# Performance work log

Measured on AMD Instinct MI355X. Metric: run time of the kernel, lower is better.

Reference implementation:

```python
import jax, jax.numpy as jnp
import numpy as np
import jax.scipy.linalg as jsl
from jax import lax

N_SAMPLES = 16384
N_COMPONENTS = 16
N_FEATURES = 128
EPS = 1e-3
MAX_DEPTH = 8
JITTER = 1e-6
LOG_2PI = float(np.log(2.0 * np.pi))


def _em_update(x, means, covs):
    # One call of update_parameters(): weights are (un-normalized) mahalanobis
    # distances computed with the OLD means/covariances; diffs for the
    # covariance update also use the OLD means (diff is computed before the
    # in-place mean assignment in the torch code).
    d = x.shape[1]
    inv = jnp.linalg.inv(covs)                      # [K,D,D]
    diff = x[:, None, :] - means[None, :, :]        # [N,K,D]
    sol = jnp.einsum('kde,nke->nkd', inv, diff)     # [N,K,D]
    w = jnp.einsum('nkd,nkd->nk', diff, sol)        # [N,K] mahalanobis dists
    sw = w.sum(axis=0)                              # [K]
    new_means = jnp.einsum('nk,nd->kd', w, x) / sw[:, None]
    outer = jnp.einsum('nk,nkd,nke->kde', w, diff, diff)
    new_covs = outer / sw[:, None, None] + JITTER * jnp.eye(d, dtype=x.dtype)
    return new_means, new_covs


def _em_loop(x, means, covs):
    # Faithful to the torch while-loop: update first, then check convergence
    # of the means (Frobenius norm) against eps, up to max_depth iterations.
    def cond(c):
        _, _, _, depth, done = c
        return jnp.logical_and(depth < MAX_DEPTH, jnp.logical_not(done))

    def body(c):
        m, cv, prev, depth, _ = c
        nm, nc = _em_update(x, m, cv)
        diff = jnp.linalg.norm(nm - prev)
        done = diff <= EPS
        return (nm, nc, nm, depth + 1, done)

    init = (means, covs, means, jnp.int32(0), jnp.bool_(False))
    m, cv, _, _, _ = lax.while_loop(cond, body, init)
    return m, cv


def _log_prob(x, means, covs):
    # MultivariateNormal.log_prob for each component, batched over K via
    # Cholesky (matching torch.distributions internals).
    d = x.shape[1]
    L = jnp.linalg.cholesky(covs)                   # [K,D,D]
    diff = x[:, None, :] - means[None, :, :]        # [N,K,D]
    # per-component triangular solve: L_k y = diff[:,k,:]^T -> y [K,D,N]
    y = jax.vmap(lambda Lk, dk: jsl.solve_triangular(Lk, dk.T, lower=True),
                 in_axes=(0, 1))(L, diff)
    maha = jnp.sum(y * y, axis=1)                   # [K,N]
    logdet = 2.0 * jnp.sum(jnp.log(jnp.diagonal(L, axis1=-2, axis2=-1)), axis=-1)  # [K]
    return -0.5 * (d * LOG_2PI + logdet[:, None] + maha)  # [K,N]


def _forward(x, means, covariances, weights):
    # torch.no_grad() EM loop -> stop_gradient on loop inputs/outputs
    m0 = lax.stop_gradient(means)
    c0 = lax.stop_gradient(covariances)
    xs = lax.stop_gradient(x)
    m_loop, c_loop = _em_loop(xs, m0, c0)
    # final update_parameters call (training path, outside no_grad)
    m_fin, c_fin = _em_update(x, m_loop, c_loop)
    logp = _log_prob(x, m_fin, c_fin)               # [K,N]
    loss = -jnp.sum(weights[:, None] * logp)
    return loss, m_fin, c_fin


def setup_inputs() -> dict:
    key = jax.random.key(0)
    k1, k2 = jax.random.split(key)
    x = jax.random.normal(k1, (N_SAMPLES, N_FEATURES), dtype=jnp.float32)
    means = jax.random.normal(k2, (N_COMPONENTS, N_FEATURES), dtype=jnp.float32)
    covariances = jnp.tile(jnp.eye(N_FEATURES, dtype=jnp.float32),
                           (N_COMPONENTS, 1, 1))
    weights = jnp.ones((N_COMPONENTS,), jnp.float32) / N_COMPONENTS
    return {"x": x, "means": means, "covariances": covariances,
            "weights": weights}


def reference(x, means, covariances, weights):
    return _forward(x, means, covariances, weights)
```

## Files before the change

kernel.cpp:

```cpp
#include <hip/hip_runtime.h>
#include <math.h>


#define NS 16384
#define DD 128
#define KC 16
#define JITTER_ 1e-6f
#define EPS2_ 1e-6f
#define LOG_2PI_ 1.8378770664093454f
#define NCHUNK 1024

typedef __attribute__((ext_vector_type(8))) short bf16x8;
typedef __attribute__((ext_vector_type(16))) float f32x16;

enum : int {
  OFF_CUR_M  = 0,
  OFF_CS     = 2048,
  OFF_T      = 528384,
  OFF_LOGDET = 530432,
  OFF_SW     = 530448,
  OFF_NUM    = 530464,
  OFF_W      = 532512,
  OFF_LOSSK  = 794656,
  OFF_DIFFSQ = 794672,
  OFF_DONE   = 794673,
  OFF_CTR    = 794674,
  OFF_XAH    = 794676,
  OFF_XAL    = 1843252,
  OFF_XBH    = 2891828,
  OFF_XBL    = 3940404,
  OFF_LBH    = 4988980,
  OFF_LBL    = 5120052,
  WS_FLOATS  = 5251124
};

__device__ __forceinline__ float bf2f(ushort u) {
  union { unsigned u; float f; } c; c.u = ((unsigned)u) << 16; return c.f;
}
__device__ __forceinline__ ushort f2bf_rne(float f) {
  union { float f; unsigned u; } c; c.f = f;
  unsigned r = c.u + 0x7fffu + ((c.u >> 16) & 1u);
  return (ushort)(r >> 16);
}
__device__ __forceinline__ ushort f2bf_trunc(float f) {
  union { float f; unsigned u; } c; c.f = f; return (ushort)(c.u >> 16);
}

__device__ __forceinline__ int swz(int r, int c) {
  return (r << 7) + ((((c >> 2) + r) & 31) << 2) + (c & 3);
}

__device__ __forceinline__ float rdlane(float v, int lane) {
  union { float f; int i; } c; c.f = v;
  c.i = __builtin_amdgcn_readlane(c.i, lane);
  return c.f;
}

__device__ __forceinline__ void frag_write(const float* Zs, ushort* LBH,
                                           ushort* LBL, int g) {
  int ll = g & 63, ks2 = (g >> 6) & 1, ec = (g >> 7) & 3, dg = (g >> 9) & 3;
  int d = 32 * dg + (ll & 31);
  int e = 32 * ec + 16 * ks2 + 8 * (ll >> 5);
  float4 z0 = *(const float4*)&Zs[d * 132 + e];
  float4 z1 = *(const float4*)&Zs[d * 132 + e + 4];
  float zv[8] = {z0.x, z0.y, z0.z, z0.w, z1.x, z1.y, z1.z, z1.w};
  ushort hh[8], lo2[8];
  #pragma unroll
  for (int j = 0; j < 8; ++j) {
    hh[j]  = f2bf_trunc(zv[j]);
    lo2[j] = f2bf_rne(zv[j] - bf2f(hh[j]));
  }
  *(ushort4*)&LBH[g * 8]     = make_ushort4(hh[0], hh[1], hh[2], hh[3]);
  *(ushort4*)&LBH[g * 8 + 4] = make_ushort4(hh[4], hh[5], hh[6], hh[7]);
  *(ushort4*)&LBL[g * 8]     = make_ushort4(lo2[0], lo2[1], lo2[2], lo2[3]);
  *(ushort4*)&LBL[g * 8 + 4] = make_ushort4(lo2[4], lo2[5], lo2[6], lo2[7]);
}

__global__ __launch_bounds__(256) void k_init_split(const float* __restrict__ x,
                                                    const float* __restrict__ means,
                                                    const float* __restrict__ covs,
                                                    float* __restrict__ ws) {
  __shared__ float xt[64 * 132];
  int b = blockIdx.x, t = threadIdx.x;
  int idx = b * 256 + t;
  for (int i = idx; i < KC * DD * DD; i += 256 * 256) ws[OFF_CS + i] = covs[i];
  if (idx < KC * DD) ws[OFF_CUR_M + idx] = means[idx];
  if (idx == 0) {
    ws[OFF_DIFFSQ] = 0.f;
    ((int*)ws)[OFF_DONE] = 0;
    ((int*)ws)[OFF_CTR]  = 0;
  }
  int n0 = b * 64;
  for (int fi = t; fi < 2048; fi += 256) {
    int n = fi >> 5, q = (fi & 31) * 4;
    *(float4*)&xt[n * 132 + q] = *(const float4*)&x[(size_t)(n0 + n) * DD + q];
  }
  __syncthreads();
  ushort* __restrict__ XAH = (ushort*)(ws + OFF_XAH);
  ushort* __restrict__ XAL = (ushort*)(ws + OFF_XAL);
  ushort* __restrict__ XBH = (ushort*)(ws + OFF_XBH);
  ushort* __restrict__ XBL = (ushort*)(ws + OFF_XBL);
  for (int s = t; s < 1024; s += 256) {
    int l = s & 63, ks = (s >> 6) & 1, ec = (s >> 7) & 3, ngl = (s >> 9) & 1;
    int nl = 32 * ngl + (l & 31);
    int e0 = 32 * ec + 16 * ks + 8 * (l >> 5);
    float vv[8];
    *(float4*)&vv[0] = *(const float4*)&xt[nl * 132 + e0];
    *(float4*)&vv[4] = *(const float4*)&xt[nl * 132 + e0 + 4];
    ushort h[8], lo[8];
    #pragma unroll
    for (int j = 0; j < 8; ++j) {
      h[j]  = f2bf_trunc(vv[j]);
      lo[j] = f2bf_rne(vv[j] - bf2f(h[j]));
    }
    size_t base = ((((size_t)((n0 >> 5) + ngl) * 4 + ec) * 2 + ks) * 64 + l) * 8;
    *(ushort4*)&XAH[base]     = make_ushort4(h[0], h[1], h[2], h[3]);
    *(ushort4*)&XAH[base + 4] = make_ushort4(h[4], h[5], h[6], h[7]);
    *(ushort4*)&XAL[base]     = make_ushort4(lo[0], lo[1], lo[2], lo[3]);
    *(ushort4*)&XAL[base + 4] = make_ushort4(lo[4], lo[5], lo[6], lo[7]);
  }
  for (int s = t; s < 1024; s += 256) {
    int l = s & 63, nbl = (s >> 6) & 3, eg = (s >> 8) & 3;
    int e = 32 * eg + (l & 31);
    int nl = 16 * nbl + 8 * (l >> 5);
    ushort h[8], lo[8];
    #pragma unroll
    for (int j = 0; j < 8; ++j) {
      float v = xt[(nl + j) * 132 + e];
      h[j]  = f2bf_trunc(v);
      lo[j] = f2bf_rne(v - bf2f(h[j]));
    }
    size_t base = (((size_t)eg * (NS / 16) + (n0 >> 4) + nbl) * 64 + l) * 8;
    *(ushort4*)&XBH[base]     = make_ushort4(h[0], h[1], h[2], h[3]);
    *(ushort4*)&XBH[base + 4] = make_ushort4(h[4], h[5], h[6], h[7]);
    *(ushort4*)&XBL[base]     = make_ushort4(lo[0], lo[1], lo[2], lo[3]);
    *(ushort4*)&XBL[base + 4] = make_ushort4(lo[4], lo[5], lo[6], lo[7]);
  }
}

__global__ __launch_bounds__(512) void k_fused(float* __restrict__ ws, float* __restrict__ dout,
                                               int guarded, int do_update, int write_out,
                                               int accum_diff, int final_pass) {
  if (guarded && ((const int*)ws)[OFF_DONE]) return;
  __shared__ float m[DD * DD];
  __shared__ float Zs[DD * 132];
  __shared__ float Ws[64 * 68];
  __shared__ float invd_s[DD];
  __shared__ float cm_s[DD], nm_s[DD];
  __shared__ float redbuf[2];
  int k = blockIdx.x, t = threadIdx.x;
  int l = t & 63, wv = t >> 6;
  float* __restrict__ CS = ws + OFF_CS + (size_t)k * DD * DD;

  if (do_update) {
    float sw = ws[OFF_SW + k];
    float inv = 1.f / sw;
    float4 s4v[8];
    #pragma unroll
    for (int it = 0; it < 8; ++it)
      s4v[it] = *(const float4*)&CS[(it * 512 + t) * 4];
    if (t < DD) {
      cm_s[t] = ws[OFF_CUR_M + k * DD + t];
      nm_s[t] = ws[OFF_NUM + k * DD + t];
    }
    __syncthreads();
    float* __restrict__ doutC = dout + 1 + KC * DD + (size_t)k * DD * DD;
    #pragma unroll
    for (int it = 0; it < 8; ++it) {
      int idx = (it * 512 + t) * 4;
      float4 s4 = s4v[it];
      int d = idx >> 7, e = idx & 127;
      float md = cm_s[d], nd = nm_s[d];
      float4 me4 = *(const float4*)&cm_s[e];
      float4 ne4 = *(const float4*)&nm_s[e];
      float4 v;
      v.x = (s4.x - md * ne4.x - nd * me4.x + sw * md * me4.x) * inv;
      v.y = (s4.y - md * ne4.y - nd * me4.y + sw * md * me4.y) * inv;
      v.z = (s4.z - md * ne4.z - nd * me4.z + sw * md * me4.z) * inv;
      v.w = (s4.w - md * ne4.w - nd * me4.w + sw * md * me4.w) * inv;
      if (d >= e && d < e + 4) (&v.x)[d - e] += JITTER_;
      *(float4*)&m[swz(d, e)] = v;
      if (write_out) *(float4*)&doutC[idx] = v;
    }
    if (t < DD) {
      float me = cm_s[t], ne = nm_s[t];
      float newm = ne * inv;
      ws[OFF_CUR_M + k * DD + t] = newm;
      if (write_out) dout[1 + k * DD + t] = newm;
      if (accum_diff) {
        float dm = newm - me;
        float s = dm * dm;
        #pragma unroll
        for (int mk2 = 1; mk2 < 64; mk2 <<= 1) s += __shfl_xor(s, mk2, 64);
        if (l == 0) redbuf[wv] = s;
      }
      ws[OFF_NUM + k * DD + t] = 0.f;
    }
    if (t == 0) {
      ws[OFF_SW + k] = 0.f;
      if (final_pass) ws[OFF_LOSSK + k] = 0.f;
    }
  } else {
    #pragma unroll
    for (int it = 0; it < 8; ++it) {
      int idx = (it * 512 + t) * 4;
      float4 c4 = *(const float4*)&CS[idx];
      *(float4*)&m[swz(idx >> 7, idx & 127)] = c4;
    }
    if (t < DD) ws[OFF_NUM + k * DD + t] = 0.f;
    if (t == 0) ws[OFF_SW + k] = 0.f;
  }
  __syncthreads();

  auto FACTOR = [&](int P) {
    int ra = P + l, rb = P + 64 + l;
    bool isA = (wv == 0);
    bool va = ra < DD, vb = rb < DD;
    float A[16], B[16];
    if (va) {
      #pragma unroll
      for (int q = 0; q < 4; ++q) {
        float4 v = *(const float4*)&m[swz(ra, P + 4 * q)];
        A[4*q+0] = v.x; A[4*q+1] = v.y; A[4*q+2] = v.z; A[4*q+3] = v.w;
      }
    }
    if (!isA && vb) {
      #pragma unroll
      for (int q = 0; q < 4; ++q) {
        float4 v = *(const float4*)&m[swz(rb, P + 4 * q)];
        B[4*q+0] = v.x; B[4*q+1] = v.y; B[4*q+2] = v.z; B[4*q+3] = v.w;
      }
    }
    #pragma unroll
    for (int jj = 0; jj < 16; ++jj) {
      float dj = rdlane(A[jj], jj);
      float inv = __builtin_amdgcn_rsqf(dj);
      inv = inv * (1.5f - 0.5f * dj * inv * inv);
      float sj = dj * inv;
      if (va) {
        if (l == jj) A[jj] = sj;
        else if (l > jj) A[jj] *= inv;
      }
      if (!isA && vb) B[jj] *= inv;
      #pragma unroll
      for (int jj2 = jj + 1; jj2 < 16; ++jj2) {
        float c = rdlane(A[jj], jj2);
        if (va && l > jj) A[jj2] -= A[jj] * c;
        if (!isA && vb) B[jj2] -= B[jj] * c;
      }
    }
    if (isA && va) {
      #pragma unroll
      for (int q = 0; q < 4; ++q)
        *(float4*)&m[swz(ra, P + 4 * q)] = make_float4(A[4*q], A[4*q+1], A[4*q+2], A[4*q+3]);
    }
    if (!isA && vb) {
      #pragma unroll
      for (int q = 0; q < 4; ++q)
        *(float4*)&m[swz(rb, P + 4 * q)] = make_float4(B[4*q], B[4*q+1], B[4*q+2], B[4*q+3]);
    }
  };
  auto TILE16 = [&](int i0, int q0, int P) {
    float acc4[4][4] = {};
    #pragma unroll
    for (int pq = 0; pq < 4; ++pq) {
      float4 a[4], b[4];
      #pragma unroll
      for (int r = 0; r < 4; ++r) a[r] = *(const float4*)&m[swz(i0 + r, P + 4 * pq)];
      #pragma unroll
      for (int c = 0; c < 4; ++c) b[c] = *(const float4*)&m[swz(q0 + c, P + 4 * pq)];
      #pragma unroll
      for (int r = 0; r < 4; ++r)
        #pragma unroll
        for (int c = 0; c < 4; ++c)
          acc4[r][c] += a[r].x * b[c].x + a[r].y * b[c].y +
                        a[r].z * b[c].z + a[r].w * b[c].w;
    }
    #pragma unroll
    for (int r = 0; r < 4; ++r) {
      float4 v = *(const float4*)&m[swz(i0 + r, q0)];
      v.x -= acc4[r][0]; v.y -= acc4[r][1]; v.z -= acc4[r][2]; v.w -= acc4[r][3];
      *(float4*)&m[swz(i0 + r, q0)] = v;
    }
  };

  if (wv < 2) FACTOR(0);
  __syncthreads();
  for (int P = 0; P < DD - 16; P += 16) {
    int C0 = P + 16;
    int nts = DD - C0;
    for (int idx = t; idx < nts; idx += 512)
      TILE16(C0 + 4 * (idx >> 2), C0 + 4 * (idx & 3), P);
    __syncthreads();
    if (wv < 2) {
      FACTOR(C0);
    } else {
      int R0 = P + 32, s = DD - R0;
      if (s > 0) {
        int nt = s >> 2, tri = (nt * (nt + 1)) >> 1;
        for (int idx = t - 128; idx < tri; idx += 384) {
          int ti = (int)(0.5f * (sqrtf(8.f * (float)idx + 1.f) - 1.f));
          while (((ti + 1) * (ti + 2)) >> 1 <= idx) ++ti;
          while ((ti * (ti + 1)) >> 1 > idx) --ti;
          int tj = idx - ((ti * (ti + 1)) >> 1);
          TILE16(R0 + 4 * ti, R0 + 4 * tj, P);
        }
      }
    }
    __syncthreads();
  }

  if (t < DD) {
    float dv = m[swz(t, t)];
    invd_s[t] = 1.f / dv;
    if (final_pass) {
      float lg = logf(dv);
      #pragma unroll
      for (int mk2 = 1; mk2 < 64; mk2 <<= 1) lg += __shfl_xor(lg, mk2, 64);
      if (l == 0) redbuf[wv] = lg;
    }
  }
  __syncthreads();
  if (t < DD) {
    int b = t >> 5, j = t & 31, r0 = 32 * b;
    float acc[32];
    #pragma unroll
    for (int i2 = 0; i2 < 32; ++i2) acc[i2] = 0.f;
    #pragma unroll
    for (int p = 0; p < 32; ++p) {
      float zp = (((p == j) ? 1.f : 0.f) - acc[p]) * invd_s[r0 + p];
      Zs[(r0 + p) * 132 + r0 + j] = zp;
      #pragma unroll
      for (int i2 = p + 1; i2 < 32; ++i2)
        acc[i2] += m[swz(r0 + i2, r0 + p)] * zp;
    }
  } else {
    for (int z = t - 128; z < 1536; z += 384) {
      int r, c;
      if (z < 1024) { r = z >> 4; c = 64 + ((z & 15) << 2); }
      else { int z2 = z - 1024; int h = z2 >> 8; int z3 = z2 & 255;
             r = h * 64 + (z3 >> 3); c = h * 64 + 32 + ((z3 & 7) << 2); }
      *(float4*)&Zs[r * 132 + c] = make_float4(0.f, 0.f, 0.f, 0.f);
    }
    if (final_pass && t == 128) ws[OFF_LOGDET + k] = 2.f * (redbuf[0] + redbuf[1]);
  }
  __syncthreads();
  {
    int h = t >> 8, i = (t >> 3) & 31, j0 = (t & 7) << 2;
    int rI = h * 64 + 32 + i, cb = h * 64;
    float ax = 0.f, ay = 0.f, az = 0.f, aw = 0.f;
    #pragma unroll
    for (int q0 = 0; q0 < 32; q0 += 4) {
      float4 a  = *(const float4*)&m[swz(rI, cb + q0)];
      float4 z0 = *(const float4*)&Zs[(cb + q0 + 0) * 132 + cb + j0];
      float4 z1 = *(const float4*)&Zs[(cb + q0 + 1) * 132 + cb + j0];
      float4 z2 = *(const float4*)&Zs[(cb + q0 + 2) * 132 + cb + j0];
      float4 z3 = *(const float4*)&Zs[(cb + q0 + 3) * 132 + cb + j0];
      ax += a.x * z0.x + a.y * z1.x + a.z * z2.x + a.w * z3.x;
      ay += a.x * z0.y + a.y * z1.y + a.z * z2.y + a.w * z3.y;
      az += a.x * z0.z + a.y * z1.z + a.z * z2.z + a.w * z3.z;
      aw += a.x * z0.w + a.y * z1.w + a.z * z2.w + a.w * z3.w;
    }
    *(float4*)&Ws[(h * 32 + i) * 68 + j0] = make_float4(ax, ay, az, aw);
  }
  __syncthreads();
  {
    int h = t >> 8, i = (t >> 3) & 31, j0 = (t & 7) << 2;
    int rI = h * 64 + 32 + i;
    float ax = 0.f, ay = 0.f, az = 0.f, aw = 0.f;
    #pragma unroll
    for (int q0 = 0; q0 < 32; q0 += 4) {
      float4 a  = *(const float4*)&Zs[rI * 132 + h * 64 + 32 + q0];
      float4 w0 = *(const float4*)&Ws[(h * 32 + q0 + 0) * 68 + j0];
      float4 w1 = *(const float4*)&Ws[(h * 32 + q0 + 1) * 68 + j0];
      float4 w2 = *(const float4*)&Ws[(h * 32 + q0 + 2) * 68 + j0];
      float4 w3 = *(const float4*)&Ws[(h * 32 + q0 + 3) * 68 + j0];
      ax += a.x * w0.x + a.y * w1.x + a.z * w2.x + a.w * w3.x;
      ay += a.x * w0.y + a.y * w1.y + a.z * w2.y + a.w * w3.y;
      az += a.x * w0.z + a.y * w1.z + a.z * w2.z + a.w * w3.z;
      aw += a.x * w0.w + a.y * w1.w + a.z * w2.w + a.w * w3.w;
    }
    *(float4*)&Zs[rI * 132 + h * 64 + j0] = make_float4(-ax, -ay, -az, -aw);
  }
  __syncthreads();
  ushort* __restrict__ LBH = (ushort*)(ws + OFF_LBH) + (size_t)k * 16384;
  ushort* __restrict__ LBL = (ushort*)(ws + OFF_LBL) + (size_t)k * 16384;
  if (t < 256) {
    int i0 = (t & 15) << 2, j0 = (t >> 4) << 2;
    float acc4[4][4] = {};
    for (int q0 = 0; q0 < 64; q0 += 4) {
      float4 a[4], b[4];
      #pragma unroll
      for (int r = 0; r < 4; ++r) a[r] = *(const float4*)&m[swz(64 + i0 + r, q0)];
      #pragma unroll
      for (int s2 = 0; s2 < 4; ++s2) b[s2] = *(const float4*)&Zs[(q0 + s2) * 132 + j0];
      #pragma unroll
      for (int r = 0; r < 4; ++r) {
        acc4[r][0] += a[r].x * b[0].x + a[r].y * b[1].x + a[r].z * b[2].x + a[r].w * b[3].x;
        acc4[r][1] += a[r].x * b[0].y + a[r].y * b[1].y + a[r].z * b[2].y + a[r].w * b[3].y;
        acc4[r][2] += a[r].x * b[0].z + a[r].y * b[1].z + a[r].z * b[2].z + a[r].w * b[3].z;
        acc4[r][3] += a[r].x * b[0].w + a[r].y * b[1].w + a[r].z * b[2].w + a[r].w * b[3].w;
      }
    }
    #pragma unroll
    for (int r = 0; r < 4; ++r)
      *(float4*)&Ws[(i0 + r) * 68 + j0] =
          make_float4(acc4[r][0], acc4[r][1], acc4[r][2], acc4[r][3]);
  } else {
    #pragma unroll
    for (int it = 0; it < 3; ++it) frag_write(Zs, LBH, LBL, (t - 256) + it * 256);
  }
  __syncthreads();
  if (t < 256) {
    int i0 = (t & 15) << 2, j0 = (t >> 4) << 2;
    float acc4[4][4] = {};
    for (int q0 = 0; q0 < 64; q0 += 4) {
      float4 a[4], b[4];
      #pragma unroll
      for (int r = 0; r < 4; ++r)
        a[r] = *(const float4*)&Zs[(64 + i0 + r) * 132 + 64 + q0];
      #pragma unroll
      for (int s2 = 0; s2 < 4; ++s2) b[s2] = *(const float4*)&Ws[(q0 + s2) * 68 + j0];
      #pragma unroll
      for (int r = 0; r < 4; ++r) {
        acc4[r][0] += a[r].x * b[0].x + a[r].y * b[1].x + a[r].z * b[2].x + a[r].w * b[3].x;
        acc4[r][1] += a[r].x * b[0].y + a[r].y * b[1].y + a[r].z * b[2].y + a[r].w * b[3].y;
        acc4[r][2] += a[r].x * b[0].z + a[r].y * b[1].z + a[r].z * b[2].z + a[r].w * b[3].z;
        acc4[r][3] += a[r].x * b[0].w + a[r].y * b[1].w + a[r].z * b[2].w + a[r].w * b[3].w;
      }
    }
    #pragma unroll
    for (int r = 0; r < 4; ++r)
      *(float4*)&Zs[(64 + i0 + r) * 132 + j0] =
          make_float4(-acc4[r][0], -acc4[r][1], -acc4[r][2], -acc4[r][3]);
  } else {
    #pragma unroll
    for (int it = 0; it < 3; ++it) {
      int r = 768 + (t - 256) + it * 256;
      int g;
      if (r < 1024) g = r;
      else { int rr = r - 1024;
             g = (2 + (rr >> 8)) * 512 + (2 + ((rr >> 7) & 1)) * 128 + (rr & 127); }
      frag_write(Zs, LBH, LBL, g);
    }
  }
  __syncthreads();
  if (t < DD) {
    const float* __restrict__ mk = ws + OFF_CUR_M + k * DD;
    float s0 = 0.f;
    for (int e = 0; e < DD; e += 4) {
      float4 z = *(const float4*)&Zs[t * 132 + e];
      s0 += z.x * mk[e] + z.y * mk[e + 1] + z.z * mk[e + 2] + z.w * mk[e + 3];
    }
    ws[OFF_T + k * DD + t] = s0;
  } else {
    for (int rr = t - 128; rr < 512; rr += 384) {
      int g = (2 + (rr >> 8)) * 512 + ((rr >> 7) & 1) * 128 + (rr & 127);
      frag_write(Zs, LBH, LBL, g);
    }
  }
  if (accum_diff && t == 0) {
    atomicAdd(&ws[OFF_DIFFSQ], redbuf[0] + redbuf[1]);
    __threadfence();
    int old = atomicAdd((int*)ws + OFF_CTR, 1);
    if ((old & (KC - 1)) == KC - 1) {
      float v = atomicAdd(&ws[OFF_DIFFSQ], 0.f);
      if (v <= EPS2_) atomicExch((int*)ws + OFF_DONE, 1);
      atomicExch(&ws[OFF_DIFFSQ], 0.f);
    }
  }
}

__global__ __launch_bounds__(256) void k_quad(float* __restrict__ ws,
                                              const float* __restrict__ wts,
                                              int guarded, int final_pass) {
  if (guarded && ((const int*)ws)[OFF_DONE]) return;
  __shared__ float warr[128];
  int k = blockIdx.y, bx = blockIdx.x, t = threadIdx.x;
  int l = t & 63, wv = t >> 6;
  int n0 = bx * 128;
  if (t < 128) ws[OFF_CS + (size_t)k * DD * DD + bx * 128 + t] = 0.f;
  const ushort* __restrict__ XAH = (const ushort*)(ws + OFF_XAH);
  const ushort* __restrict__ XAL = (const ushort*)(ws + OFF_XAL);
  const ushort* __restrict__ LBH = (const ushort*)(ws + OFF_LBH) + (size_t)k * 16384;
  const ushort* __restrict__ LBL = (const ushort*)(ws + OFF_LBL) + (size_t)k * 16384;
  f32x16 acc[4] = {};
  size_t ng4 = (size_t)(4 * bx + wv) * 4;
  #pragma unroll
  for (int ec = 0; ec < 4; ++ec) {
    #pragma unroll
    for (int ks = 0; ks < 2; ++ks) {
      size_t aoff = (((ng4 + ec) * 2 + ks) * 64 + l) * 8;
      bf16x8 ah = *(const bf16x8*)&XAH[aoff];
      bf16x8 al = *(const bf16x8*)&XAL[aoff];
      #pragma unroll
      for (int dg = 0; dg < 4; ++dg) {
        size_t boff = ((((size_t)dg * 4 + ec) * 2 + ks) * 64 + l) * 8;
        bf16x8 bh = *(const bf16x8*)&LBH[boff];
        bf16x8 bl = *(const bf16x8*)&LBL[boff];
        acc[dg] = __builtin_amdgcn_mfma_f32_32x32x16_bf16(ah, bh, acc[dg], 0, 0, 0);
        acc[dg] = __builtin_amdgcn_mfma_f32_32x32x16_bf16(ah, bl, acc[dg], 0, 0, 0);
        acc[dg] = __builtin_amdgcn_mfma_f32_32x32x16_bf16(al, bh, acc[dg], 0, 0, 0);
      }
    }
  }
  float tv[4];
  #pragma unroll
  for (int c = 0; c < 4; ++c) tv[c] = ws[OFF_T + k * DD + 32 * c + (l & 31)];
  float part[16];
  #pragma unroll
  for (int r = 0; r < 16; ++r) {
    float s = 0.f;
    #pragma unroll
    for (int c = 0; c < 4; ++c) { float d = acc[c][r] - tv[c]; s += d * d; }
    part[r] = s;
  }
  #pragma unroll
  for (int mk2 = 1; mk2 < 32; mk2 <<= 1)
    #pragma unroll
    for (int r = 0; r < 16; ++r) part[r] += __shfl_xor(part[r], mk2, 64);
  int h = l >> 5;
  if ((l & 31) < 16) {
    int r = l & 31;
    int row = (r & 3) + 8 * (r >> 2) + 4 * h + 32 * wv;
    ws[OFF_W + k * NS + n0 + row] = part[r];
    if (final_pass) warr[row] = part[r];
  }
  if (final_pass) {
    __syncthreads();
    if (t < 64) {
      float s = warr[t] + warr[t + 64];
      #pragma unroll
      for (int mk2 = 1; mk2 < 64; mk2 <<= 1) s += __shfl_xor(s, mk2, 64);
      if (t == 0) atomicAdd(&ws[OFF_LOSSK + k], 0.5f * wts[k] * s);
    }
  }
}

__global__ __launch_bounds__(256, 4) void k_scatter(float* __restrict__ ws, int guarded) {
  if (guarded && ((const int*)ws)[OFF_DONE]) return;
  __shared__ float Sred[8192];
  int id = blockIdx.x, t = threadIdx.x;
  int xcd = id & 7, j = id >> 3;
  int chunk = xcd + 8 * (j & 1);
  int dg = (j >> 1) & 3;
  int k = j >> 3;
  int l = t & 63, wv = t >> 6;
  const ushort* __restrict__ XBH = (const ushort*)(ws + OFF_XBH);
  const ushort* __restrict__ XBL = (const ushort*)(ws + OFF_XBL);
  const float* __restrict__ wp = ws + OFF_W + k * NS + chunk * NCHUNK;
  f32x16 acc[4] = {};
  int nb0 = chunk * (NCHUNK / 16) + wv * (NCHUNK / 64);
  int ko = (l >> 5) * 8;
  float zsum = 0.f, wsum = 0.f;
  size_t aoff = (((size_t)dg * (NS / 16) + nb0) * 64 + l) * 8;
  bf16x8 th = *(const bf16x8*)&XBH[aoff];
  bf16x8 tl = *(const bf16x8*)&XBL[aoff];
  float4 w0 = *(const float4*)&wp[16 * (wv * (NCHUNK / 64)) + ko];
  float4 w1 = *(const float4*)&wp[16 * (wv * (NCHUNK / 64)) + ko + 4];
  for (int st = 0; st < NCHUNK / 64; ++st) {
    int stn = (st + 1) & (NCHUNK / 64 - 1);
    size_t aoffn = (((size_t)dg * (NS / 16) + nb0 + stn) * 64 + l) * 8;
    bf16x8 thn = *(const bf16x8*)&XBH[aoffn];
    bf16x8 tln = *(const bf16x8*)&XBL[aoffn];
    int wbn = 16 * (wv * (NCHUNK / 64) + stn) + ko;
    float4 w0n = *(const float4*)&wp[wbn];
    float4 w1n = *(const float4*)&wp[wbn + 4];
    float wj[8] = {w0.x, w0.y, w0.z, w0.w, w1.x, w1.y, w1.z, w1.w};
    bf16x8 ah, al;
    #pragma unroll
    for (int jj = 0; jj < 8; ++jj) {
      float xf = bf2f((ushort)th[jj]) + bf2f((ushort)tl[jj]);
      float zf = wj[jj] * xf;
      zsum += zf;
      union { float f; unsigned u; } cz; cz.f = zf;
      ah[jj] = (short)(ushort)(cz.u >> 16);
      union { unsigned u; float f; } ch; ch.u = cz.u & 0xffff0000u;
      al[jj] = (short)f2bf_rne(zf - ch.f);
    }
    if (dg == 0 && (l & 31) == 0) {
      #pragma unroll
      for (int jj = 0; jj < 8; ++jj) wsum += wj[jj];
    }
    #pragma unroll
    for (int eg = 0; eg < 4; ++eg) {
      size_t boff = (((size_t)eg * (NS / 16) + nb0 + st) * 64 + l) * 8;
      bf16x8 bh = *(const bf16x8*)&XBH[boff];
      bf16x8 bl = *(const bf16x8*)&XBL[boff];
      acc[eg] = __builtin_amdgcn_mfma_f32_32x32x16_bf16(ah, bh, acc[eg], 0, 0, 0);
      acc[eg] = __builtin_amdgcn_mfma_f32_32x32x16_bf16(ah, bl, acc[eg], 0, 0, 0);
      acc[eg] = __builtin_amdgcn_mfma_f32_32x32x16_bf16(al, bh, acc[eg], 0, 0, 0);
    }
    th = thn; tl = tln; w0 = w0n; w1 = w1n;
  }
  zsum += __shfl_xor(zsum, 32, 64);
  if (l < 32) atomicAdd(&ws[OFF_NUM + k * DD + 32 * dg + l], zsum);
  if (dg == 0) {
    wsum += __shfl_xor(wsum, 32, 64);
    if (l == 0) atomicAdd(&ws[OFF_SW + k], wsum);
  }
  float* __restrict__ S = ws + OFF_CS + (size_t)k * DD * DD;
  #pragma unroll
  for (int p = 0; p < 2; ++p) {
    if (p) __syncthreads();
    #pragma unroll
    for (int egL = 0; egL < 2; ++egL)
      #pragma unroll
      for (int r = 0; r < 16; ++r)
        Sred[(wv * 2 + egL) * 1024 + r * 64 + l] = acc[2 * p + egL][r];
    __syncthreads();
    #pragma unroll
    for (int i = 0; i < 8; ++i) {
      int idx = i * 256 + t;
      int ll = idx & 63, r = (idx >> 6) & 15, egL = idx >> 10;
      int base = egL * 1024 + r * 64 + ll;
      float s = Sred[base] + Sred[base + 2048] + Sred[base + 4096] + Sred[base + 6144];
      int h = ll >> 5;
      int drow = 32 * dg + (r & 3) + 8 * (r >> 2) + 4 * h;
      int e = 32 * (2 * p + egL) + (ll & 31);
      atomicAdd(&S[drow * DD + e], s);
    }
  }
}

__global__ void k_lossfin(const float* __restrict__ weights, const float* __restrict__ ws,
                          float* __restrict__ dout) {
  if (threadIdx.x == 0 && blockIdx.x == 0) {
    float base = 0.f;
    for (int k = 0; k < KC; ++k)
      base += weights[k] * 0.5f * (float)NS * ((float)DD * LOG_2PI_ + ws[OFF_LOGDET + k])
            + ws[OFF_LOSSK + k];
    dout[0] = base;
  }
}

extern "C" void kernel_launch(void* const* d_in, const int* in_sizes, int n_in,
                              void* d_out, int out_size, void* d_ws, size_t ws_size,
                              hipStream_t stream) {
  const float* x       = (const float*)d_in[0];
  const float* means   = (const float*)d_in[1];
  const float* covs    = (const float*)d_in[2];
  const float* weights = (const float*)d_in[3];
  float* out = (float*)d_out;
  float* ws  = (float*)d_ws;

  hipLaunchKernelGGL(k_init_split, dim3(NS / 64), dim3(256), 0, stream, x, means, covs, ws);
  hipLaunchKernelGGL(k_fused, dim3(16), dim3(512), 0, stream, ws, out, 0, 0, 0, 0, 0);

  for (int u = 0; u < 8; ++u) {
    hipLaunchKernelGGL(k_quad,    dim3(128, 16), dim3(256), 0, stream, ws, weights, 1, 0);
    hipLaunchKernelGGL(k_scatter, dim3(1024), dim3(256), 0, stream, ws, 1);
    hipLaunchKernelGGL(k_fused,   dim3(16), dim3(512), 0, stream, ws, out, 1, 1, 0, 1, 0);
  }

  hipLaunchKernelGGL(k_quad,    dim3(128, 16), dim3(256), 0, stream, ws, weights, 0, 0);
  hipLaunchKernelGGL(k_scatter, dim3(1024), dim3(256), 0, stream, ws, 0);
  hipLaunchKernelGGL(k_fused,   dim3(16), dim3(512), 0, stream, ws, out, 0, 1, 1, 0, 1);
  hipLaunchKernelGGL(k_quad,    dim3(128, 16), dim3(256), 0, stream, ws, weights, 0, 1);
  hipLaunchKernelGGL(k_lossfin, dim3(1), dim3(64), 0, stream, weights, ws, out);
}
```

Measured before the change: 871.2 us.

## Retile Cholesky trailing updates and triangular inverse for better register reuse

```diff
diff --git a/kernel.cpp b/kernel.cpp
--- a/kernel.cpp
+++ b/kernel.cpp
@@ -260,50 +260,74 @@
         *(float4*)&m[swz(rb, P + 4 * q)] = make_float4(B[4*q], B[4*q+1], B[4*q+2], B[4*q+3]);
     }
   };
-  auto TILE16 = [&](int i0, int q0, int P) {
-    float acc4[4][4] = {};
+  auto TILE8 = [&](int i0, int q0, int P) {
+    float acc8[8][8] = {};
     #pragma unroll
     for (int pq = 0; pq < 4; ++pq) {
-      float4 a[4], b[4];
-      #pragma unroll
-      for (int r = 0; r < 4; ++r) a[r] = *(const float4*)&m[swz(i0 + r, P + 4 * pq)];
-      #pragma unroll
-      for (int c = 0; c < 4; ++c) b[c] = *(const float4*)&m[swz(q0 + c, P + 4 * pq)];
-      #pragma unroll
-      for (int r = 0; r < 4; ++r)
+      float4 a[8], b[8];
+      #pragma unroll
+      for (int r = 0; r < 8; ++r) a[r] = *(const float4*)&m[swz(i0 + r, P + 4 * pq)];
+      #pragma unroll
+      for (int c = 0; c < 8; ++c) b[c] = *(const float4*)&m[swz(q0 + c, P + 4 * pq)];
+      #pragma unroll
+      for (int r = 0; r < 8; ++r)
         #pragma unroll
-        for (int c = 0; c < 4; ++c)
-          acc4[r][c] += a[r].x * b[c].x + a[r].y * b[c].y +
+        for (int c = 0; c < 8; ++c)
+          acc8[r][c] += a[r].x * b[c].x + a[r].y * b[c].y +
                         a[r].z * b[c].z + a[r].w * b[c].w;
     }
     #pragma unroll
-    for (int r = 0; r < 4; ++r) {
-      float4 v = *(const float4*)&m[swz(i0 + r, q0)];
-      v.x -= acc4[r][0]; v.y -= acc4[r][1]; v.z -= acc4[r][2]; v.w -= acc4[r][3];
-      *(float4*)&m[swz(i0 + r, q0)] = v;
-    }
+    for (int r = 0; r < 8; ++r)
+      #pragma unroll
+      for (int cq = 0; cq < 2; ++cq) {
+        float4 v = *(const float4*)&m[swz(i0 + r, q0 + 4 * cq)];
+        v.x -= acc8[r][4*cq+0]; v.y -= acc8[r][4*cq+1];
+        v.z -= acc8[r][4*cq+2]; v.w -= acc8[r][4*cq+3];
+        *(float4*)&m[swz(i0 + r, q0 + 4 * cq)] = v;
+      }
   };
 
   if (wv < 2) FACTOR(0);
   __syncthreads();
   for (int P = 0; P < DD - 16; P += 16) {
     int C0 = P + 16;
-    int nts = DD - C0;
-    for (int idx = t; idx < nts; idx += 512)
-      TILE16(C0 + 4 * (idx >> 2), C0 + 4 * (idx & 3), P);
+    int nts = ((DD - C0) >> 1) * 4;
+    for (int idx = t; idx < nts; idx += 512) {
+      int r0 = C0 + 2 * (idx >> 2), q0 = C0 + 4 * (idx & 3);
+      float acc2[2][4] = {};
+      #pragma unroll
+      for (int pq = 0; pq < 4; ++pq) {
+        float4 a0 = *(const float4*)&m[swz(r0, P + 4 * pq)];
+        float4 a1 = *(const float4*)&m[swz(r0 + 1, P + 4 * pq)];
+        float4 b[4];
+        #pragma unroll
+        for (int c = 0; c < 4; ++c) b[c] = *(const float4*)&m[swz(q0 + c, P + 4 * pq)];
+        #pragma unroll
+        for (int c = 0; c < 4; ++c) {
+          acc2[0][c] += a0.x * b[c].x + a0.y * b[c].y + a0.z * b[c].z + a0.w * b[c].w;
+          acc2[1][c] += a1.x * b[c].x + a1.y * b[c].y + a1.z * b[c].z + a1.w * b[c].w;
+        }
+      }
+      float4 v0 = *(const float4*)&m[swz(r0, q0)];
+      v0.x -= acc2[0][0]; v0.y -= acc2[0][1]; v0.z -= acc2[0][2]; v0.w -= acc2[0][3];
+      *(float4*)&m[swz(r0, q0)] = v0;
+      float4 v1 = *(const float4*)&m[swz(r0 + 1, q0)];
+      v1.x -= acc2[1][0]; v1.y -= acc2[1][1]; v1.z -= acc2[1][2]; v1.w -= acc2[1][3];
+      *(float4*)&m[swz(r0 + 1, q0)] = v1;
+    }
     __syncthreads();
     if (wv < 2) {
       FACTOR(C0);
     } else {
       int R0 = P + 32, s = DD - R0;
       if (s > 0) {
-        int nt = s >> 2, tri = (nt * (nt + 1)) >> 1;
+        int nt = s >> 3, tri = (nt * (nt + 1)) >> 1;
         for (int idx = t - 128; idx < tri; idx += 384) {
           int ti = (int)(0.5f * (sqrtf(8.f * (float)idx + 1.f) - 1.f));
           while (((ti + 1) * (ti + 2)) >> 1 <= idx) ++ti;
           while ((ti * (ti + 1)) >> 1 > idx) --ti;
           int tj = idx - ((ti * (ti + 1)) >> 1);
-          TILE16(R0 + 4 * ti, R0 + 4 * tj, P);
+          TILE8(R0 + 8 * ti, R0 + 8 * tj, P);
         }
       }
     }
@@ -321,8 +345,14 @@
     }
   }
   __syncthreads();
-  if (t < DD) {
-    int b = t >> 5, j = t & 31, r0 = 32 * b;
+  if (wv < 4) {
+    int j = l & 31, r0 = 32 * wv, row = r0 + (l & 31);
+    float M[32];
+    #pragma unroll
+    for (int q = 0; q < 8; ++q) {
+      float4 v = *(const float4*)&m[swz(row, r0 + 4 * q)];
+      M[4*q+0] = v.x; M[4*q+1] = v.y; M[4*q+2] = v.z; M[4*q+3] = v.w;
+    }
     float acc[32];
     #pragma unroll
     for (int i2 = 0; i2 < 32; ++i2) acc[i2] = 0.f;
@@ -332,17 +362,17 @@
       Zs[(r0 + p) * 132 + r0 + j] = zp;
       #pragma unroll
       for (int i2 = p + 1; i2 < 32; ++i2)
-        acc[i2] += m[swz(r0 + i2, r0 + p)] * zp;
+        acc[i2] += rdlane(M[p], i2) * zp;
     }
   } else {
-    for (int z = t - 128; z < 1536; z += 384) {
+    for (int z = t - 256; z < 1536; z += 256) {
       int r, c;
       if (z < 1024) { r = z >> 4; c = 64 + ((z & 15) << 2); }
       else { int z2 = z - 1024; int h = z2 >> 8; int z3 = z2 & 255;
              r = h * 64 + (z3 >> 3); c = h * 64 + 32 + ((z3 & 7) << 2); }
       *(float4*)&Zs[r * 132 + c] = make_float4(0.f, 0.f, 0.f, 0.f);
     }
-    if (final_pass && t == 128) ws[OFF_LOGDET + k] = 2.f * (redbuf[0] + redbuf[1]);
+    if (final_pass && t == 256) ws[OFF_LOGDET + k] = 2.f * (redbuf[0] + redbuf[1]);
   }
   __syncthreads();
   {
@@ -385,17 +415,17 @@
   __syncthreads();
   ushort* __restrict__ LBH = (ushort*)(ws + OFF_LBH) + (size_t)k * 16384;
   ushort* __restrict__ LBL = (ushort*)(ws + OFF_LBL) + (size_t)k * 16384;
-  if (t < 256) {
-    int i0 = (t & 15) << 2, j0 = (t >> 4) << 2;
-    float acc4[4][4] = {};
+  if (t < 128) {
+    int i0 = (t >> 4) << 3, j0 = (t & 15) << 2;
+    float acc4[8][4] = {};
     for (int q0 = 0; q0 < 64; q0 += 4) {
-      float4 a[4], b[4];
-      #pragma unroll
-      for (int r = 0; r < 4; ++r) a[r] = *(const float4*)&m[swz(64 + i0 + r, q0)];
+      float4 a[8], b[4];
+      #pragma unroll
+      for (int r = 0; r < 8; ++r) a[r] = *(const float4*)&m[swz(64 + i0 + r, q0)];
       #pragma unroll
       for (int s2 = 0; s2 < 4; ++s2) b[s2] = *(const float4*)&Zs[(q0 + s2) * 132 + j0];
       #pragma unroll
-      for (int r = 0; r < 4; ++r) {
+      for (int r = 0; r < 8; ++r) {
         acc4[r][0] += a[r].x * b[0].x + a[r].y * b[1].x + a[r].z * b[2].x + a[r].w * b[3].x;
         acc4[r][1] += a[r].x * b[0].y + a[r].y * b[1].y + a[r].z * b[2].y + a[r].w * b[3].y;
         acc4[r][2] += a[r].x * b[0].z + a[r].y * b[1].z + a[r].z * b[2].z + a[r].w * b[3].z;
@@ -403,26 +433,26 @@
       }
     }
     #pragma unroll
-    for (int r = 0; r < 4; ++r)
+    for (int r = 0; r < 8; ++r)
       *(float4*)&Ws[(i0 + r) * 68 + j0] =
           make_float4(acc4[r][0], acc4[r][1], acc4[r][2], acc4[r][3]);
   } else {
     #pragma unroll
-    for (int it = 0; it < 3; ++it) frag_write(Zs, LBH, LBL, (t - 256) + it * 256);
-  }
-  __syncthreads();
-  if (t < 256) {
-    int i0 = (t & 15) << 2, j0 = (t >> 4) << 2;
-    float acc4[4][4] = {};
+    for (int it = 0; it < 2; ++it) frag_write(Zs, LBH, LBL, (t - 128) + it * 384);
+  }
+  __syncthreads();
+  if (t < 128) {
+    int i0 = (t >> 4) << 3, j0 = (t & 15) << 2;
+    float acc4[8][4] = {};
     for (int q0 = 0; q0 < 64; q0 += 4) {
-      float4 a[4], b[4];
-      #pragma unroll
-      for (int r = 0; r < 4; ++r)
+      float4 a[8], b[4];
+      #pragma unroll
+      for (int r = 0; r < 8; ++r)
         a[r] = *(const float4*)&Zs[(64 + i0 + r) * 132 + 64 + q0];
       #pragma unroll
       for (int s2 = 0; s2 < 4; ++s2) b[s2] = *(const float4*)&Ws[(q0 + s2) * 68 + j0];
       #pragma unroll
-      for (int r = 0; r < 4; ++r) {
+      for (int r = 0; r < 8; ++r) {
         acc4[r][0] += a[r].x * b[0].x + a[r].y * b[1].x + a[r].z * b[2].x + a[r].w * b[3].x;
         acc4[r][1] += a[r].x * b[0].y + a[r].y * b[1].y + a[r].z * b[2].y + a[r].w * b[3].y;
         acc4[r][2] += a[r].x * b[0].z + a[r].y * b[1].z + a[r].z * b[2].z + a[r].w * b[3].z;
@@ -430,13 +460,13 @@
       }
     }
     #pragma unroll
-    for (int r = 0; r < 4; ++r)
+    for (int r = 0; r < 8; ++r)
       *(float4*)&Zs[(64 + i0 + r) * 132 + j0] =
           make_float4(-acc4[r][0], -acc4[r][1], -acc4[r][2], -acc4[r][3]);
   } else {
     #pragma unroll
-    for (int it = 0; it < 3; ++it) {
-      int r = 768 + (t - 256) + it * 256;
+    for (int it = 0; it < 2; ++it) {
+      int r = 768 + (t - 128) + it * 384;
       int g;
       if (r < 1024) g = r;
       else { int rr = r - 1024;
```

After: 844.1 us. -3.1%, faster.
